# Optimization experiments

Measured on AMD Instinct MI355X. Metric: run time of the kernel, lower is better.

The kernel has to match this reference:

```python
import jax, jax.numpy as jnp
import numpy as np

TEMP = 0.1
EPS = 0.5
N, D, P = 8192, 128, 1


def setup_inputs() -> dict:
    key = jax.random.key(0)
    k1, k2 = jax.random.split(key)
    return {
        "embeddings": jax.random.normal(k1, (N, D), dtype=jnp.float32),
        "properties": jax.random.uniform(k2, (N, P), dtype=jnp.float32),
    }


def reference(embeddings, properties):
    n = embeddings.shape[0]
    # L2-normalize rows, cosine similarity scaled by temperature
    e = embeddings / jnp.linalg.norm(embeddings, axis=1, keepdims=True)
    sim = (e @ e.T) / TEMP  # [N, N]

    # mask from property distances; comparison is non-differentiable in torch,
    # so stop_gradient keeps the jax graph identical (and avoids sqrt(0) nans)
    props = jax.lax.stop_gradient(properties)
    pd2 = jnp.sum((props[:, None, :] - props[None, :, :]) ** 2, axis=-1)  # [N, N]
    # torch.cdist(p=2) gives sqrt(pd2); code then takes .sqrt() again -> pd2**0.25
    prop_dists = jnp.sqrt(jnp.sqrt(pd2)) + 1e-8
    mask = (prop_dists < EPS).astype(sim.dtype)

    eye = jnp.eye(n, dtype=bool)
    mask = jnp.where(eye, 0.0, mask)          # fill_diagonal_(0)
    logits = jnp.where(eye, -1e9, sim)        # fill_diagonal_(-1e9)
    log_probs = jax.nn.log_softmax(logits, axis=1)

    # fused masked per-row mean of -log_probs over positives, then mean over
    # rows that have at least one positive (replaces the python loop)
    counts = mask.sum(axis=1)                      # [N]
    valid = counts > 0
    per_row = -(mask * log_probs).sum(axis=1) / jnp.maximum(counts, 1.0)
    n_valid = valid.sum()
    loss = jnp.where(
        n_valid > 0,
        jnp.sum(jnp.where(valid, per_row, 0.0)) / jnp.maximum(n_valid, 1).astype(per_row.dtype),
        jnp.asarray(0.0, dtype=per_row.dtype),
    )
    return loss
```

## Files before the change

### kernel.cpp

```cpp
#include <hip/hip_runtime.h>
#include <hip/hip_bf16.h>

#define N_ROWS 8192
#define DIM 128

typedef short v8s  __attribute__((ext_vector_type(8)));
typedef float v16f __attribute__((ext_vector_type(16)));
typedef float v2f  __attribute__((ext_vector_type(2)));
typedef unsigned int u32;

constexpr int NS = 16;
constexpr int CW = N_ROWS / NS;
constexpr int NSLOT = NS;
constexpr int TILE_J = 32;
constexpr int NT = CW / TILE_J;
constexpr int TB = TILE_J * DIM * 2;
constexpr int BI = 256;
constexpr int NRB = N_ROWS / 64;
constexpr float T2 = 0.0625f;
constexpr float C1 = 14.426950408889634f;

#define GLDS(gptr, lptr, sz)                                                   \
  __builtin_amdgcn_global_load_lds(                                            \
      (const __attribute__((address_space(1))) u32*)(gptr),                    \
      (__attribute__((address_space(3))) u32*)(lptr), sz, 0, 0)

__device__ __forceinline__ unsigned short f2bf(float f) {
  __hip_bfloat16 h = __float2bfloat16(f);
  return __builtin_bit_cast(unsigned short, h);
}

__global__ __launch_bounds__(256) void knorm(const float* __restrict__ emb,
                                             unsigned short* __restrict__ ebf,
                                             int* __restrict__ cnt) {
  if (blockIdx.x == 0 && threadIdx.x == 0) cnt[0] = 0;
  const int row  = blockIdx.x * 4 + (threadIdx.x >> 6);
  const int lane = threadIdx.x & 63;
  const float2 v = *reinterpret_cast<const float2*>(emb + (size_t)row * DIM + lane * 2);
  float ss = fmaf(v.x, v.x, v.y * v.y);
#pragma unroll
  for (int off = 32; off > 0; off >>= 1) ss += __shfl_xor(ss, off);
  const float rn = 1.0f / sqrtf(ss);
  const unsigned int packed =
      (unsigned int)f2bf(v.x * rn) | ((unsigned int)f2bf(v.y * rn) << 16);
  *reinterpret_cast<unsigned int*>(ebf + (size_t)row * DIM + lane * 2) = packed;
}

__global__ __launch_bounds__(512, 4) void kmain(const unsigned short* __restrict__ ebf,
                                                const float* __restrict__ props,
                                                float* __restrict__ part) {
  const int tid  = threadIdx.x;
  const int lane = tid & 63;
  const int w    = tid >> 6;
  const int r31  = lane & 31;
  const int hi   = lane >> 5;
  const int i0   = blockIdx.x * BI;
  const int iw0  = i0 + w * 32;
  const int jbase = blockIdx.y * CW;

  __shared__ __align__(1024) char sA[4 * TB + CW * 4];
  char* sprops = sA + 4 * TB;

  const int icol = iw0 + r31;

  v8s bfr[8];
#pragma unroll
  for (int kk = 0; kk < 8; ++kk)
    bfr[kk] = *reinterpret_cast<const v8s*>(ebf + (size_t)icol * DIM + kk * 16 + hi * 8);
  const float pc = props[icol];

  GLDS(props + jbase + tid, sprops + w * 256, 4);

  auto stageA = [&](char* base, int tile) {
    const int jrow0 = jbase + tile * TILE_J;
    const int row   = w * 4 + (lane >> 4);
    const int colb  = ((lane & 15) << 4) ^ ((row & 7) << 4);
    GLDS(ebf + (size_t)(jrow0 + row) * DIM + (colb >> 1), base + w * 1024, 16);
  };

  v2f es2 = {0.f, 0.f}, ms2 = {0.f, 0.f}, ct2 = {0.f, 0.f};
  const int rswz = (r31 & 7) << 4;
  const v2f c1v = {C1, C1}, mc1v = {-C1, -C1}, pc2 = {pc, pc};

  auto compute = [&](const char* base, int tt) {
    const int jrow0 = jbase + tt * TILE_J;
    v8s af[8];
#pragma unroll
    for (int kk = 0; kk < 8; ++kk)
      af[kk] = *reinterpret_cast<const v8s*>(
          base + r31 * 256 + ((kk * 32 + hi * 16) ^ rswz));

    v16f acc = {0.f, 0.f, 0.f, 0.f, 0.f, 0.f, 0.f, 0.f,
                0.f, 0.f, 0.f, 0.f, 0.f, 0.f, 0.f, 0.f};
#pragma unroll
    for (int kk = 0; kk < 8; ++kk)
      acc = __builtin_amdgcn_mfma_f32_32x32x16_bf16(af[kk], bfr[kk], acc, 0, 0, 0);

    if ((unsigned)(jrow0 - i0) < (unsigned)BI) {
#pragma unroll
      for (int r = 0; r < 8; ++r) {
        const int row0 = ((2 * r) & 3) + 8 * (r >> 1) + 4 * hi;
        const v2f pj2  = *reinterpret_cast<const v2f*>(
            sprops + ((size_t)tt * 32 + row0) * 4);
        const v2f dot2 = {acc[2 * r], acc[2 * r + 1]};
        const v2f arg  = __builtin_elementwise_fma(dot2, c1v, mc1v);
        const float ex0 = __builtin_amdgcn_exp2f(arg.x);
        const float ex1 = __builtin_amdgcn_exp2f(arg.y);
        const int jr0 = jrow0 + row0;
        const bool neq0 = (jr0 != icol), neq1 = (jr0 + 1 != icol);
        const v2f exv = {neq0 ? ex0 : 0.f, neq1 ? ex1 : 0.f};
        es2 += exv;
        const v2f d = pc2 - pj2, dsq = d * d;
        const v2f msk = {(neq0 && dsq.x < T2) ? 1.f : 0.f,
                         (neq1 && dsq.y < T2) ? 1.f : 0.f};
        ct2 += msk;
        ms2 = __builtin_elementwise_fma(msk, dot2, ms2);
      }
    } else {
#pragma unroll
      for (int r = 0; r < 8; ++r) {
        const int row0 = ((2 * r) & 3) + 8 * (r >> 1) + 4 * hi;
        const v2f pj2  = *reinterpret_cast<const v2f*>(
            sprops + ((size_t)tt * 32 + row0) * 4);
        const v2f dot2 = {acc[2 * r], acc[2 * r + 1]};
        const v2f arg  = __builtin_elementwise_fma(dot2, c1v, mc1v);
        const v2f exv  = {__builtin_amdgcn_exp2f(arg.x), __builtin_amdgcn_exp2f(arg.y)};
        es2 += exv;
        const v2f d = pc2 - pj2, dsq = d * d;
        const v2f msk = {(dsq.x < T2) ? 1.f : 0.f, (dsq.y < T2) ? 1.f : 0.f};
        ct2 += msk;
        ms2 = __builtin_elementwise_fma(msk, dot2, ms2);
      }
    }
  };

  const int phase = (blockIdx.x * 5) & (NT - 1);
  stageA(sA + 0 * TB, phase);
  stageA(sA + 1 * TB, (phase + 1) & (NT - 1));
  __syncthreads();

  for (int t = 0; t < NT; t += 2) {
    const int tt0 = (t + phase) & (NT - 1);
    const int tt1 = (t + 1 + phase) & (NT - 1);
    if (t + 2 < NT) {
      stageA(sA + ((t + 2) & 3) * TB, (tt0 + 2) & (NT - 1));
      stageA(sA + ((t + 3) & 3) * TB, (tt1 + 2) & (NT - 1));
    }
    compute(sA + (t & 3) * TB, tt0);
    compute(sA + ((t + 1) & 3) * TB, tt1);
    __syncthreads();
  }

  float es = es2.x + es2.y, ms = ms2.x + ms2.y, ct = ct2.x + ct2.y;
  es += __shfl_xor(es, 32);
  ms += __shfl_xor(ms, 32);
  ct += __shfl_xor(ct, 32);

  if (hi == 0) {
    float* p0 = part + (size_t)blockIdx.y * 3 * N_ROWS;
    p0[icol]              = es;
    p0[N_ROWS + icol]     = ms;
    p0[2 * N_ROWS + icol] = ct;
  }
}

__global__ __launch_bounds__(64) void kreduce(const float* __restrict__ part,
                                              volatile float* __restrict__ bs,
                                              volatile float* __restrict__ bc,
                                              int* __restrict__ cnt,
                                              float* __restrict__ out) {
  const int row = blockIdx.x * 64 + threadIdx.x;
  float es = 0.f, ms = 0.f, ct = 0.f;
#pragma unroll
  for (int sp = 0; sp < NSLOT; ++sp) {
    const float* p0 = part + (size_t)sp * 3 * N_ROWS;
    es += p0[row];
    ms += p0[N_ROWS + row];
    ct += p0[2 * N_ROWS + row];
  }
  const float lse = 10.0f + logf(es);
  const float per = (ct * lse - 10.0f * ms) / fmaxf(ct, 1.0f);
  float val = (ct > 0.f) ? per : 0.f;
  float vld = (ct > 0.f) ? 1.f : 0.f;
#pragma unroll
  for (int off = 32; off > 0; off >>= 1) {
    val += __shfl_xor(val, off);
    vld += __shfl_xor(vld, off);
  }

  __shared__ int ticket;
  if (threadIdx.x == 0) {
    bs[blockIdx.x] = val;
    bc[blockIdx.x] = vld;
    __threadfence();
    ticket = atomicAdd(cnt, 1);
  }
  __syncthreads();
  if (ticket == NRB - 1) {
    __threadfence();
    const int l = threadIdx.x;
    float s = bs[l] + bs[l + 64];
    float c = bc[l] + bc[l + 64];
#pragma unroll
    for (int off = 32; off > 0; off >>= 1) {
      s += __shfl_xor(s, off);
      c += __shfl_xor(c, off);
    }
    if (l == 0) out[0] = (c > 0.f) ? (s / c) : 0.f;
  }
}

extern "C" void kernel_launch(void* const* d_in, const int* in_sizes, int n_in,
                              void* d_out, int out_size, void* d_ws, size_t ws_size,
                              hipStream_t stream) {
  const float* emb   = (const float*)d_in[0];
  const float* props = (const float*)d_in[1];
  float* out = (float*)d_out;

  unsigned short* ebf = (unsigned short*)d_ws;
  const size_t EBF_BYTES  = (size_t)N_ROWS * DIM * 2;
  const size_t PART_BYTES = (size_t)NSLOT * 3 * N_ROWS * 4;
  float* part = (float*)((char*)d_ws + EBF_BYTES);
  float* bs   = (float*)((char*)d_ws + EBF_BYTES + PART_BYTES);
  float* bc   = bs + NRB;
  int*   cnt  = (int*)(bc + NRB);

  knorm<<<N_ROWS / 4, 256, 0, stream>>>(emb, ebf, cnt);
  kmain<<<dim3(N_ROWS / BI, NS), 512, 0, stream>>>(ebf, props, part);
  kreduce<<<NRB, 64, 0, stream>>>(part, bs, bc, cnt, out);
}
```

Measured before the change: 47.98 us.

## Compute two 32-column i-tiles per wave to reuse each A fragment

Each wave now owns 64 i-columns (two 32x32 MFMA tiles) instead of 32, and the block shrinks from 512 to 256 threads. Each A fragment read from LDS feeds two MFMAs, which halves LDS reads per MFMA and gives more independent MFMA work per wave. Staging is split across fewer threads, so each thread issues two loads per tile. The cost is roughly double the register use for B fragments and accumulators, and fewer waves per block, which may lower occupancy and latency hiding.

Result: slower. 50.10 us (+4.4%).

```diff
diff --git a/kernel.cpp b/kernel.cpp
--- a/kernel.cpp
+++ b/kernel.cpp
@@ -46,41 +46,53 @@
   *reinterpret_cast<unsigned int*>(ebf + (size_t)row * DIM + lane * 2) = packed;
 }
 
-__global__ __launch_bounds__(512, 4) void kmain(const unsigned short* __restrict__ ebf,
-                                                const float* __restrict__ props,
-                                                float* __restrict__ part) {
+__global__ __launch_bounds__(256) void kmain(const unsigned short* __restrict__ ebf,
+                                             const float* __restrict__ props,
+                                             float* __restrict__ part) {
   const int tid  = threadIdx.x;
   const int lane = tid & 63;
   const int w    = tid >> 6;
   const int r31  = lane & 31;
   const int hi   = lane >> 5;
   const int i0   = blockIdx.x * BI;
-  const int iw0  = i0 + w * 32;
+  const int iw0  = i0 + w * 64;
   const int jbase = blockIdx.y * CW;
 
   __shared__ __align__(1024) char sA[4 * TB + CW * 4];
   char* sprops = sA + 4 * TB;
 
-  const int icol = iw0 + r31;
-
-  v8s bfr[8];
-#pragma unroll
-  for (int kk = 0; kk < 8; ++kk)
-    bfr[kk] = *reinterpret_cast<const v8s*>(ebf + (size_t)icol * DIM + kk * 16 + hi * 8);
-  const float pc = props[icol];
-
-  GLDS(props + jbase + tid, sprops + w * 256, 4);
+  const int icolA = iw0 + r31;
+  const int icolB = iw0 + 32 + r31;
+
+  v8s bfrA[8], bfrB[8];
+#pragma unroll
+  for (int kk = 0; kk < 8; ++kk) {
+    bfrA[kk] = *reinterpret_cast<const v8s*>(ebf + (size_t)icolA * DIM + kk * 16 + hi * 8);
+    bfrB[kk] = *reinterpret_cast<const v8s*>(ebf + (size_t)icolB * DIM + kk * 16 + hi * 8);
+  }
+  const float pcA = props[icolA];
+  const float pcB = props[icolB];
+
+#pragma unroll
+  for (int r = 0; r < 2; ++r)
+    GLDS(props + jbase + r * 256 + tid, sprops + r * 1024 + w * 256, 4);
 
   auto stageA = [&](char* base, int tile) {
     const int jrow0 = jbase + tile * TILE_J;
-    const int row   = w * 4 + (lane >> 4);
-    const int colb  = ((lane & 15) << 4) ^ ((row & 7) << 4);
-    GLDS(ebf + (size_t)(jrow0 + row) * DIM + (colb >> 1), base + w * 1024, 16);
+#pragma unroll
+    for (int q = 0; q < 2; ++q) {
+      const int row  = q * 16 + w * 4 + (lane >> 4);
+      const int colb = ((lane & 15) << 4) ^ ((row & 7) << 4);
+      GLDS(ebf + (size_t)(jrow0 + row) * DIM + (colb >> 1),
+           base + q * 4096 + w * 1024, 16);
+    }
   };
 
-  v2f es2 = {0.f, 0.f}, ms2 = {0.f, 0.f}, ct2 = {0.f, 0.f};
+  v2f esA = {0.f, 0.f}, msA = {0.f, 0.f}, ctA = {0.f, 0.f};
+  v2f esB = {0.f, 0.f}, msB = {0.f, 0.f}, ctB = {0.f, 0.f};
   const int rswz = (r31 & 7) << 4;
-  const v2f c1v = {C1, C1}, mc1v = {-C1, -C1}, pc2 = {pc, pc};
+  const v2f c1v = {C1, C1}, mc1v = {-C1, -C1};
+  const v2f pcA2 = {pcA, pcA}, pcB2 = {pcB, pcB};
 
   auto compute = [&](const char* base, int tt) {
     const int jrow0 = jbase + tt * TILE_J;
@@ -90,11 +102,14 @@
       af[kk] = *reinterpret_cast<const v8s*>(
           base + r31 * 256 + ((kk * 32 + hi * 16) ^ rswz));
 
-    v16f acc = {0.f, 0.f, 0.f, 0.f, 0.f, 0.f, 0.f, 0.f,
-                0.f, 0.f, 0.f, 0.f, 0.f, 0.f, 0.f, 0.f};
-#pragma unroll
-    for (int kk = 0; kk < 8; ++kk)
-      acc = __builtin_amdgcn_mfma_f32_32x32x16_bf16(af[kk], bfr[kk], acc, 0, 0, 0);
+    v16f accA = {0.f, 0.f, 0.f, 0.f, 0.f, 0.f, 0.f, 0.f,
+                 0.f, 0.f, 0.f, 0.f, 0.f, 0.f, 0.f, 0.f};
+    v16f accB = accA;
+#pragma unroll
+    for (int kk = 0; kk < 8; ++kk) {
+      accA = __builtin_amdgcn_mfma_f32_32x32x16_bf16(af[kk], bfrA[kk], accA, 0, 0, 0);
+      accB = __builtin_amdgcn_mfma_f32_32x32x16_bf16(af[kk], bfrB[kk], accB, 0, 0, 0);
+    }
 
     if ((unsigned)(jrow0 - i0) < (unsigned)BI) {
 #pragma unroll
@@ -102,19 +117,33 @@
         const int row0 = ((2 * r) & 3) + 8 * (r >> 1) + 4 * hi;
         const v2f pj2  = *reinterpret_cast<const v2f*>(
             sprops + ((size_t)tt * 32 + row0) * 4);
-        const v2f dot2 = {acc[2 * r], acc[2 * r + 1]};
-        const v2f arg  = __builtin_elementwise_fma(dot2, c1v, mc1v);
-        const float ex0 = __builtin_amdgcn_exp2f(arg.x);
-        const float ex1 = __builtin_amdgcn_exp2f(arg.y);
         const int jr0 = jrow0 + row0;
-        const bool neq0 = (jr0 != icol), neq1 = (jr0 + 1 != icol);
-        const v2f exv = {neq0 ? ex0 : 0.f, neq1 ? ex1 : 0.f};
-        es2 += exv;
-        const v2f d = pc2 - pj2, dsq = d * d;
-        const v2f msk = {(neq0 && dsq.x < T2) ? 1.f : 0.f,
-                         (neq1 && dsq.y < T2) ? 1.f : 0.f};
-        ct2 += msk;
-        ms2 = __builtin_elementwise_fma(msk, dot2, ms2);
+        {
+          const v2f dot2 = {accA[2 * r], accA[2 * r + 1]};
+          const v2f arg  = __builtin_elementwise_fma(dot2, c1v, mc1v);
+          const bool neq0 = (jr0 != icolA), neq1 = (jr0 + 1 != icolA);
+          const v2f exv = {neq0 ? __builtin_amdgcn_exp2f(arg.x) : 0.f,
+                           neq1 ? __builtin_amdgcn_exp2f(arg.y) : 0.f};
+          esA += exv;
+          const v2f d = pcA2 - pj2, dsq = d * d;
+          const v2f msk = {(neq0 && dsq.x < T2) ? 1.f : 0.f,
+                           (neq1 && dsq.y < T2) ? 1.f : 0.f};
+          ctA += msk;
+          msA = __builtin_elementwise_fma(msk, dot2, msA);
+        }
+        {
+          const v2f dot2 = {accB[2 * r], accB[2 * r + 1]};
+          const v2f arg  = __builtin_elementwise_fma(dot2, c1v, mc1v);
+          const bool neq0 = (jr0 != icolB), neq1 = (jr0 + 1 != icolB);
+          const v2f exv = {neq0 ? __builtin_amdgcn_exp2f(arg.x) : 0.f,
+                           neq1 ? __builtin_amdgcn_exp2f(arg.y) : 0.f};
+          esB += exv;
+          const v2f d = pcB2 - pj2, dsq = d * d;
+          const v2f msk = {(neq0 && dsq.x < T2) ? 1.f : 0.f,
+                           (neq1 && dsq.y < T2) ? 1.f : 0.f};
+          ctB += msk;
+          msB = __builtin_elementwise_fma(msk, dot2, msB);
+        }
       }
     } else {
 #pragma unroll
@@ -122,14 +151,26 @@
         const int row0 = ((2 * r) & 3) + 8 * (r >> 1) + 4 * hi;
         const v2f pj2  = *reinterpret_cast<const v2f*>(
             sprops + ((size_t)tt * 32 + row0) * 4);
-        const v2f dot2 = {acc[2 * r], acc[2 * r + 1]};
-        const v2f arg  = __builtin_elementwise_fma(dot2, c1v, mc1v);
-        const v2f exv  = {__builtin_amdgcn_exp2f(arg.x), __builtin_amdgcn_exp2f(arg.y)};
-        es2 += exv;
-        const v2f d = pc2 - pj2, dsq = d * d;
-        const v2f msk = {(dsq.x < T2) ? 1.f : 0.f, (dsq.y < T2) ? 1.f : 0.f};
-        ct2 += msk;
-        ms2 = __builtin_elementwise_fma(msk, dot2, ms2);
+        {
+          const v2f dot2 = {accA[2 * r], accA[2 * r + 1]};
+          const v2f arg  = __builtin_elementwise_fma(dot2, c1v, mc1v);
+          const v2f exv  = {__builtin_amdgcn_exp2f(arg.x), __builtin_amdgcn_exp2f(arg.y)};
+          esA += exv;
+          const v2f d = pcA2 - pj2, dsq = d * d;
+          const v2f msk = {(dsq.x < T2) ? 1.f : 0.f, (dsq.y < T2) ? 1.f : 0.f};
+          ctA += msk;
+          msA = __builtin_elementwise_fma(msk, dot2, msA);
+        }
+        {
+          const v2f dot2 = {accB[2 * r], accB[2 * r + 1]};
+          const v2f arg  = __builtin_elementwise_fma(dot2, c1v, mc1v);
+          const v2f exv  = {__builtin_amdgcn_exp2f(arg.x), __builtin_amdgcn_exp2f(arg.y)};
+          esB += exv;
+          const v2f d = pcB2 - pj2, dsq = d * d;
+          const v2f msk = {(dsq.x < T2) ? 1.f : 0.f, (dsq.y < T2) ? 1.f : 0.f};
+          ctB += msk;
+          msB = __builtin_elementwise_fma(msk, dot2, msB);
+        }
       }
     }
   };
@@ -151,16 +192,19 @@
     __syncthreads();
   }
 
-  float es = es2.x + es2.y, ms = ms2.x + ms2.y, ct = ct2.x + ct2.y;
-  es += __shfl_xor(es, 32);
-  ms += __shfl_xor(ms, 32);
-  ct += __shfl_xor(ct, 32);
+  float esa = esA.x + esA.y, msa = msA.x + msA.y, cta = ctA.x + ctA.y;
+  float esb = esB.x + esB.y, msb = msB.x + msB.y, ctb = ctB.x + ctB.y;
+  esa += __shfl_xor(esa, 32);  msa += __shfl_xor(msa, 32);  cta += __shfl_xor(cta, 32);
+  esb += __shfl_xor(esb, 32);  msb += __shfl_xor(msb, 32);  ctb += __shfl_xor(ctb, 32);
 
   if (hi == 0) {
     float* p0 = part + (size_t)blockIdx.y * 3 * N_ROWS;
-    p0[icol]              = es;
-    p0[N_ROWS + icol]     = ms;
-    p0[2 * N_ROWS + icol] = ct;
+    p0[icolA]              = esa;
+    p0[N_ROWS + icolA]     = msa;
+    p0[2 * N_ROWS + icolA] = cta;
+    p0[icolB]              = esb;
+    p0[N_ROWS + icolB]     = msb;
+    p0[2 * N_ROWS + icolB] = ctb;
   }
 }
 
@@ -226,6 +270,6 @@
   int*   cnt  = (int*)(bc + NRB);
 
   knorm<<<N_ROWS / 4, 256, 0, stream>>>(emb, ebf, cnt);
-  kmain<<<dim3(N_ROWS / BI, NS), 512, 0, stream>>>(ebf, props, part);
+  kmain<<<dim3(N_ROWS / BI, NS), 256, 0, stream>>>(ebf, props, part);
   kreduce<<<NRB, 64, 0, stream>>>(part, bs, bc, cnt, out);
 }
```
